# Optimization experiments

Hardware: AMD Instinct MI355X
Metric: run time of the kernel (lower is better)

Reference implementation:

```python
import jax, jax.numpy as jnp
from jax import lax
import numpy as np

EPS = 1e-5
TOPK_RATIO = 0.6

def _bn(y, gamma, beta, mean, var):
    # inference-mode BatchNorm3d over channel axis 1
    scale = gamma / jnp.sqrt(var + EPS)
    return (y - mean[None, :, None, None, None]) * scale[None, :, None, None, None] + beta[None, :, None, None, None]

def setup_inputs() -> dict:
    key = jax.random.key(0)
    ks = jax.random.split(key, 8)
    B, C, D, H, W = 4, 64, 16, 64, 64
    C8 = max(4, C // 8)  # bottleneck channels = 8
    x = jax.random.normal(ks[0], (B, C, D, H, W), dtype=jnp.float32)
    # depthwise conv weight, OIDHW with I=1 (groups=C), kernel (1,5,5)
    w_dw = jax.random.normal(ks[1], (C, 1, 1, 5, 5), dtype=jnp.float32) * 0.05
    bn1_gamma = jnp.ones((C,), jnp.float32)
    bn1_beta = jnp.zeros((C,), jnp.float32)
    bn1_mean = jax.random.normal(ks[2], (C,), jnp.float32) * 0.1
    bn1_var = jax.random.uniform(ks[3], (C,), jnp.float32, 0.5, 1.5)
    # pointwise 1x1x1 convs as matrices
    w_pw1 = jax.random.normal(ks[4], (C8, C), jnp.float32) * 0.05
    b_pw1 = jnp.zeros((C8,), jnp.float32)
    bn2_gamma = jnp.ones((C8,), jnp.float32)
    bn2_beta = jnp.zeros((C8,), jnp.float32)
    bn2_mean = jax.random.normal(ks[5], (C8,), jnp.float32) * 0.1
    bn2_var = jax.random.uniform(ks[6], (C8,), jnp.float32, 0.5, 1.5)
    w_pw2 = jax.random.normal(ks[7], (C, C8), jnp.float32) * 0.05
    b_pw2 = jnp.zeros((C,), jnp.float32)
    alpha = jnp.ones((), jnp.float32)
    return {"x": x, "w_dw": w_dw,
            "bn1_gamma": bn1_gamma, "bn1_beta": bn1_beta, "bn1_mean": bn1_mean, "bn1_var": bn1_var,
            "w_pw1": w_pw1, "b_pw1": b_pw1,
            "bn2_gamma": bn2_gamma, "bn2_beta": bn2_beta, "bn2_mean": bn2_mean, "bn2_var": bn2_var,
            "w_pw2": w_pw2, "b_pw2": b_pw2, "alpha": alpha}

def reference(x, w_dw, bn1_gamma, bn1_beta, bn1_mean, bn1_var,
              w_pw1, b_pw1, bn2_gamma, bn2_beta, bn2_mean, bn2_var,
              w_pw2, b_pw2, alpha):
    B, C, D, H, W = x.shape
    # branch1: depthwise conv3d (1,5,5), pad (0,2,2) + BN + SiLU
    y1 = lax.conv_general_dilated(
        x, w_dw, window_strides=(1, 1, 1),
        padding=((0, 0), (2, 2), (2, 2)),
        dimension_numbers=("NCDHW", "OIDHW", "NCDHW"),
        feature_group_count=C)
    y1 = jax.nn.silu(_bn(y1, bn1_gamma, bn1_beta, bn1_mean, bn1_var))
    # branch2: 1x1 conv -> BN -> SiLU -> 1x1 conv
    y2 = jnp.einsum("oc,bcdhw->bodhw", w_pw1, x) + b_pw1[None, :, None, None, None]
    y2 = jax.nn.silu(_bn(y2, bn2_gamma, bn2_beta, bn2_mean, bn2_var))
    y2 = jnp.einsum("oc,bcdhw->bodhw", w_pw2, y2) + b_pw2[None, :, None, None, None]
    attn = y1 * y2
    # channel-wise top-k threshold per spatial location
    k = max(1, int(TOPK_RATIO * C))
    attn_cl = jnp.moveaxis(attn, 1, -1)  # (B,D,H,W,C)
    thr = lax.top_k(attn_cl, k)[0][..., -1]  # k-th largest, (B,D,H,W)
    mask = (attn >= thr[:, None, :, :, :]).astype(attn.dtype)
    return x + alpha * (attn * mask)
```

## Files before the change

### kernel.cpp

```cpp
#include <hip/hip_runtime.h>
#include <hip/hip_fp16.h>

#define C  64
#define C8 8
#define EPSV 1e-5f

__device__ __forceinline__ float silu_f(float v) {
    return v * (1.f / (1.f + __expf(-v)));
}

__global__ __launch_bounds__(256) void fused_kernel(
    const float* __restrict__ x, const float* __restrict__ w_dw,
    const float* __restrict__ g1, const float* __restrict__ be1,
    const float* __restrict__ mu1, const float* __restrict__ va1,
    const float* __restrict__ w1, const float* __restrict__ b1,
    const float* __restrict__ g2, const float* __restrict__ be2,
    const float* __restrict__ mu2, const float* __restrict__ va2,
    const float* __restrict__ w2, const float* __restrict__ b2,
    const float* __restrict__ alphap, float* __restrict__ out)
{
    __shared__ __align__(16) __half y1s[C * 256];
    __shared__ __align__(16) __half xs [C * 256];

    const int blk = blockIdx.x;
    const int hb = blk & 15;
    const int d  = (blk >> 4) & 15;
    const int b  = blk >> 8;
    const int h0 = hb * 4;
    const int tid = threadIdx.x;

    {
        const int c     = tid >> 2;
        const int strip = tid & 3;
        const int w16   = strip * 16;
        const int q     = w16 >> 2;
        const int csw   = (c & 7) * 8;

        float wk[25];
#pragma unroll
        for (int i = 0; i < 25; ++i) wk[i] = w_dw[c * 25 + i];
        const float scale = g1[c] * rsqrtf(va1[c] + EPSV);
        const float shift = be1[c] - mu1[c] * scale;
        const long xbase = ((long)(b * C + c) * 16 + d) * 4096;

        float acc[4][16];
#pragma unroll
        for (int i = 0; i < 4; ++i)
#pragma unroll
            for (int ow = 0; ow < 16; ++ow) acc[i][ow] = 0.f;

#pragma unroll
        for (int j = 0; j < 8; ++j) {
            const int r = h0 + j - 2;
            if (r >= 0 && r < 64) {
                const float4* rowp = (const float4*)(x + xbase + r * 64);
                const float4 z = make_float4(0.f, 0.f, 0.f, 0.f);
                float4 u0 = (q > 0)  ? rowp[q - 1] : z;
                float4 u1 = rowp[q];
                float4 u2 = rowp[q + 1];
                float4 u3 = rowp[q + 2];
                float4 u4 = rowp[q + 3];
                float4 u5 = (q < 12) ? rowp[q + 4] : z;
                float vals[24] = {u0.x,u0.y,u0.z,u0.w, u1.x,u1.y,u1.z,u1.w,
                                  u2.x,u2.y,u2.z,u2.w, u3.x,u3.y,u3.z,u3.w,
                                  u4.x,u4.y,u4.z,u4.w, u5.x,u5.y,u5.z,u5.w};
                if (j >= 2 && j <= 5) {
                    const int i = j - 2;
                    const int chunkbase = i * 8 + 2 * strip;
#pragma unroll
                    for (int t = 0; t < 2; ++t) {
                        const int p = (chunkbase + t) ^ (c & 7);
                        union { __half2 h[4]; float4 f; } u;
#pragma unroll
                        for (int m = 0; m < 4; ++m)
                            u.h[m] = __floats2half2_rn(vals[4 + t * 8 + 2 * m],
                                                       vals[4 + t * 8 + 2 * m + 1]);
                        *(float4*)&xs[c * 256 + p * 8] = u.f;
                    }
                }
#pragma unroll
                for (int i = 0; i < 4; ++i) {
                    if (i <= j && (j - i) <= 4) {
                        const int kr = j - i;
#pragma unroll
                        for (int kc = 0; kc < 5; ++kc) {
                            const float kw = wk[kr * 5 + kc];
#pragma unroll
                            for (int ow = 0; ow < 16; ++ow)
                                acc[i][ow] += kw * vals[ow + kc + 2];
                        }
                    }
                }
            }
        }
#pragma unroll
        for (int i = 0; i < 4; ++i) {
            float o[16];
#pragma unroll
            for (int ow = 0; ow < 16; ++ow)
                o[ow] = silu_f(acc[i][ow] * scale + shift);
            const int chunkbase = i * 8 + 2 * strip;
#pragma unroll
            for (int t = 0; t < 2; ++t) {
                const int p = (chunkbase + t) ^ (c & 7);
                union { __half2 h[4]; float4 f; } u;
#pragma unroll
                for (int m = 0; m < 4; ++m)
                    u.h[m] = __floats2half2_rn(o[t * 8 + 2 * m], o[t * 8 + 2 * m + 1]);
                *(float4*)&y1s[c * 256 + p * 8] = u.f;
            }
        }
    }
    __syncthreads();

    {
        const int loc = tid;

        float s1[C8];
#pragma unroll
        for (int o = 0; o < C8; ++o) s1[o] = 0.f;
#pragma unroll
        for (int c = 0; c < C; ++c) {
            const float xc = __half2float(xs[c * 256 + (loc ^ ((c & 7) << 3))]);
#pragma unroll
            for (int o = 0; o < C8; ++o) s1[o] += w1[o * C + c] * xc;
        }
        float hh[C8];
#pragma unroll
        for (int o = 0; o < C8; ++o) {
            const float sc = g2[o] * rsqrtf(va2[o] + EPSV);
            hh[o] = silu_f((s1[o] + b1[o] - mu2[o]) * sc + be2[o]);
        }

        float a[C], t[C];
#pragma unroll
        for (int c = 0; c < C; ++c) {
            const float y1v = __half2float(y1s[c * 256 + (loc ^ ((c & 7) << 3))]);
            float y2 = b2[c];
#pragma unroll
            for (int o = 0; o < C8; ++o) y2 += w2[c * C8 + o] * hh[o];
            const float av = y1v * y2;
            a[c] = av;
            t[c] = av;
        }

#pragma unroll
        for (int k = 2; k <= 64; k <<= 1) {
#pragma unroll
            for (int j = k >> 1; j > 0; j >>= 1) {
#pragma unroll
                for (int i = 0; i < 64; ++i) {
                    const int l = i ^ j;
                    if (l > i) {
                        const float u = t[i], v = t[l];
                        const float mn = fminf(u, v), mx = fmaxf(u, v);
                        if ((i & k) == 0) { t[i] = mn; t[l] = mx; }
                        else              { t[i] = mx; t[l] = mn; }
                    }
                }
            }
        }
        const float thr = t[26];
        const float alpha = alphap[0];

        const int rg = d * 4096 + (h0 + (tid >> 6)) * 64 + (tid & 63);
        float* op = out + (long)b * (C * 65536) + rg;

#pragma unroll
        for (int c = 0; c < C; ++c) {
            const float xc = __half2float(xs[c * 256 + (loc ^ ((c & 7) << 3))]);
            const float av = a[c];
            op[(long)c * 65536] = xc + ((av >= thr) ? alpha * av : 0.f);
        }
    }
}

extern "C" void kernel_launch(void* const* d_in, const int* in_sizes, int n_in,
                              void* d_out, int out_size, void* d_ws, size_t ws_size,
                              hipStream_t stream) {
    const float* x    = (const float*)d_in[0];
    const float* w_dw = (const float*)d_in[1];
    const float* g1   = (const float*)d_in[2];
    const float* be1  = (const float*)d_in[3];
    const float* mu1  = (const float*)d_in[4];
    const float* va1  = (const float*)d_in[5];
    const float* w1   = (const float*)d_in[6];
    const float* b1   = (const float*)d_in[7];
    const float* g2   = (const float*)d_in[8];
    const float* be2  = (const float*)d_in[9];
    const float* mu2  = (const float*)d_in[10];
    const float* va2  = (const float*)d_in[11];
    const float* w2   = (const float*)d_in[12];
    const float* b2   = (const float*)d_in[13];
    const float* alp  = (const float*)d_in[14];
    float* out = (float*)d_out;

    fused_kernel<<<1024, 256, 0, stream>>>(
        x, w_dw, g1, be1, mu1, va1, w1, b1, g2, be2, mu2, va2, w2, b2, alp, out);
}
```

Before: 219.2 us.

## Cut registers and LDS: drop x staging, recompute attention, weights in LDS

Removes the fp16 shared-memory copy of x and rereads x from global memory (likely L2-resident) in the pointwise and output phases. The depthwise weights move from per-thread registers into a shared table. The attention values are recomputed in the output loop instead of being kept in a second 64-entry register array. Together with launch_bounds(256,4), this aims to lower VGPR and LDS use for higher occupancy. The trade is extra global loads and recomputed FMAs. Reading x at fp32 instead of from the fp16 copy also changes numerics slightly.

After: 386.2 us. 76.2% more time.

```diff
diff --git a/kernel.cpp b/kernel.cpp
--- a/kernel.cpp
+++ b/kernel.cpp
@@ -9,7 +9,7 @@
     return v * (1.f / (1.f + __expf(-v)));
 }
 
-__global__ __launch_bounds__(256) void fused_kernel(
+__global__ __launch_bounds__(256, 4) void fused_kernel(
     const float* __restrict__ x, const float* __restrict__ w_dw,
     const float* __restrict__ g1, const float* __restrict__ be1,
     const float* __restrict__ mu1, const float* __restrict__ va1,
@@ -20,7 +20,7 @@
     const float* __restrict__ alphap, float* __restrict__ out)
 {
     __shared__ __align__(16) __half y1s[C * 256];
-    __shared__ __align__(16) __half xs [C * 256];
+    __shared__ float wt[C * 25];
 
     const int blk = blockIdx.x;
     const int hb = blk & 15;
@@ -29,16 +29,15 @@
     const int h0 = hb * 4;
     const int tid = threadIdx.x;
 
+    for (int i = tid; i < C * 25; i += 256) wt[i] = w_dw[i];
+    __syncthreads();
+
     {
         const int c     = tid >> 2;
         const int strip = tid & 3;
         const int w16   = strip * 16;
         const int q     = w16 >> 2;
-        const int csw   = (c & 7) * 8;
 
-        float wk[25];
-#pragma unroll
-        for (int i = 0; i < 25; ++i) wk[i] = w_dw[c * 25 + i];
         const float scale = g1[c] * rsqrtf(va1[c] + EPSV);
         const float shift = be1[c] - mu1[c] * scale;
         const long xbase = ((long)(b * C + c) * 16 + d) * 4096;
@@ -64,27 +63,14 @@
                 float vals[24] = {u0.x,u0.y,u0.z,u0.w, u1.x,u1.y,u1.z,u1.w,
                                   u2.x,u2.y,u2.z,u2.w, u3.x,u3.y,u3.z,u3.w,
                                   u4.x,u4.y,u4.z,u4.w, u5.x,u5.y,u5.z,u5.w};
-                if (j >= 2 && j <= 5) {
-                    const int i = j - 2;
-                    const int chunkbase = i * 8 + 2 * strip;
-#pragma unroll
-                    for (int t = 0; t < 2; ++t) {
-                        const int p = (chunkbase + t) ^ (c & 7);
-                        union { __half2 h[4]; float4 f; } u;
-#pragma unroll
-                        for (int m = 0; m < 4; ++m)
-                            u.h[m] = __floats2half2_rn(vals[4 + t * 8 + 2 * m],
-                                                       vals[4 + t * 8 + 2 * m + 1]);
-                        *(float4*)&xs[c * 256 + p * 8] = u.f;
-                    }
-                }
 #pragma unroll
                 for (int i = 0; i < 4; ++i) {
                     if (i <= j && (j - i) <= 4) {
                         const int kr = j - i;
+                        const float* wrow = &wt[c * 25 + kr * 5];
 #pragma unroll
                         for (int kc = 0; kc < 5; ++kc) {
-                            const float kw = wk[kr * 5 + kc];
+                            const float kw = wrow[kc];
 #pragma unroll
                             for (int ow = 0; ow < 16; ++ow)
                                 acc[i][ow] += kw * vals[ow + kc + 2];
@@ -93,6 +79,7 @@
                 }
             }
         }
+        const int csw = (c & 7);
 #pragma unroll
         for (int i = 0; i < 4; ++i) {
             float o[16];
@@ -102,7 +89,7 @@
             const int chunkbase = i * 8 + 2 * strip;
 #pragma unroll
             for (int t = 0; t < 2; ++t) {
-                const int p = (chunkbase + t) ^ (c & 7);
+                const int p = (chunkbase + t) ^ csw;
                 union { __half2 h[4]; float4 f; } u;
 #pragma unroll
                 for (int m = 0; m < 4; ++m)
@@ -115,13 +102,15 @@
 
     {
         const int loc = tid;
+        const int rg  = d * 4096 + (h0 + (tid >> 6)) * 64 + (tid & 63);
+        const long xoff = (long)b * (C * 65536) + rg;
 
         float s1[C8];
 #pragma unroll
         for (int o = 0; o < C8; ++o) s1[o] = 0.f;
 #pragma unroll
         for (int c = 0; c < C; ++c) {
-            const float xc = __half2float(xs[c * 256 + (loc ^ ((c & 7) << 3))]);
+            const float xc = x[xoff + (long)c * 65536];
 #pragma unroll
             for (int o = 0; o < C8; ++o) s1[o] += w1[o * C + c] * xc;
         }
@@ -132,16 +121,14 @@
             hh[o] = silu_f((s1[o] + b1[o] - mu2[o]) * sc + be2[o]);
         }
 
-        float a[C], t[C];
+        float t[C];
 #pragma unroll
         for (int c = 0; c < C; ++c) {
             const float y1v = __half2float(y1s[c * 256 + (loc ^ ((c & 7) << 3))]);
             float y2 = b2[c];
 #pragma unroll
             for (int o = 0; o < C8; ++o) y2 += w2[c * C8 + o] * hh[o];
-            const float av = y1v * y2;
-            a[c] = av;
-            t[c] = av;
+            t[c] = y1v * y2;
         }
 
 #pragma unroll
@@ -163,13 +150,16 @@
         const float thr = t[26];
         const float alpha = alphap[0];
 
-        const int rg = d * 4096 + (h0 + (tid >> 6)) * 64 + (tid & 63);
-        float* op = out + (long)b * (C * 65536) + rg;
+        float* op = out + xoff;
 
 #pragma unroll
         for (int c = 0; c < C; ++c) {
-            const float xc = __half2float(xs[c * 256 + (loc ^ ((c & 7) << 3))]);
-            const float av = a[c];
+            const float y1v = __half2float(y1s[c * 256 + (loc ^ ((c & 7) << 3))]);
+            float y2 = b2[c];
+#pragma unroll
+            for (int o = 0; o < C8; ++o) y2 += w2[c * C8 + o] * hh[o];
+            const float av = y1v * y2;
+            const float xc = x[xoff + (long)c * 65536];
             op[(long)c * 65536] = xc + ((av >= thr) ? alpha * av : 0.f);
         }
     }
```

## Warp-specialize fused kernel into producer/consumer halves with double-buffered LDS

Applied to the files above, without the earlier changes.

Each block now runs 512 threads and covers four consecutive 4-row tiles. The first 256 threads compute the depthwise conv, BN and SiLU into one of two LDS buffers, while the other 256 threads handle the pointwise branch, top-k threshold and output store for the previous tile. The depthwise weights are staged in shared memory, and the consumer recomputes y2 at store time instead of keeping a second 64-entry array. This is meant to overlap the load-bound conv stage with the compute-heavy sort stage. In exchange it uses four times fewer blocks (256), doubles LDS per block, adds a pipeline fill and drain step, and introduces block-wide syncs every step.

Result: slower. 225.9 us (+3.1%).

```diff
diff --git a/kernel.cpp b/kernel.cpp
--- a/kernel.cpp
+++ b/kernel.cpp
@@ -3,13 +3,14 @@
 
 #define C  64
 #define C8 8
+#define NB 4
 #define EPSV 1e-5f
 
 __device__ __forceinline__ float silu_f(float v) {
     return v * (1.f / (1.f + __expf(-v)));
 }
 
-__global__ __launch_bounds__(256) void fused_kernel(
+__global__ __launch_bounds__(512) void fused_kernel(
     const float* __restrict__ x, const float* __restrict__ w_dw,
     const float* __restrict__ g1, const float* __restrict__ be1,
     const float* __restrict__ mu1, const float* __restrict__ va1,
@@ -19,159 +20,177 @@
     const float* __restrict__ w2, const float* __restrict__ b2,
     const float* __restrict__ alphap, float* __restrict__ out)
 {
-    __shared__ __align__(16) __half y1s[C * 256];
-    __shared__ __align__(16) __half xs [C * 256];
+    __shared__ __align__(16) __half y1s[2][C * 256];
+    __shared__ __align__(16) __half xs [2][C * 256];
+    __shared__ float wt[C * 25];
 
     const int blk = blockIdx.x;
-    const int hb = blk & 15;
-    const int d  = (blk >> 4) & 15;
-    const int b  = blk >> 8;
-    const int h0 = hb * 4;
+    const int hq  = blk & 3;
+    const int d   = (blk >> 2) & 15;
+    const int b   = blk >> 6;
     const int tid = threadIdx.x;
 
-    {
-        const int c     = tid >> 2;
-        const int strip = tid & 3;
-        const int w16   = strip * 16;
-        const int q     = w16 >> 2;
-        const int csw   = (c & 7) * 8;
-
-        float wk[25];
-#pragma unroll
-        for (int i = 0; i < 25; ++i) wk[i] = w_dw[c * 25 + i];
-        const float scale = g1[c] * rsqrtf(va1[c] + EPSV);
-        const float shift = be1[c] - mu1[c] * scale;
-        const long xbase = ((long)(b * C + c) * 16 + d) * 4096;
-
-        float acc[4][16];
-#pragma unroll
-        for (int i = 0; i < 4; ++i)
-#pragma unroll
-            for (int ow = 0; ow < 16; ++ow) acc[i][ow] = 0.f;
-
-#pragma unroll
-        for (int j = 0; j < 8; ++j) {
-            const int r = h0 + j - 2;
-            if (r >= 0 && r < 64) {
-                const float4* rowp = (const float4*)(x + xbase + r * 64);
-                const float4 z = make_float4(0.f, 0.f, 0.f, 0.f);
-                float4 u0 = (q > 0)  ? rowp[q - 1] : z;
-                float4 u1 = rowp[q];
-                float4 u2 = rowp[q + 1];
-                float4 u3 = rowp[q + 2];
-                float4 u4 = rowp[q + 3];
-                float4 u5 = (q < 12) ? rowp[q + 4] : z;
-                float vals[24] = {u0.x,u0.y,u0.z,u0.w, u1.x,u1.y,u1.z,u1.w,
-                                  u2.x,u2.y,u2.z,u2.w, u3.x,u3.y,u3.z,u3.w,
-                                  u4.x,u4.y,u4.z,u4.w, u5.x,u5.y,u5.z,u5.w};
-                if (j >= 2 && j <= 5) {
-                    const int i = j - 2;
-                    const int chunkbase = i * 8 + 2 * strip;
-#pragma unroll
-                    for (int t = 0; t < 2; ++t) {
-                        const int p = (chunkbase + t) ^ (c & 7);
-                        union { __half2 h[4]; float4 f; } u;
-#pragma unroll
-                        for (int m = 0; m < 4; ++m)
-                            u.h[m] = __floats2half2_rn(vals[4 + t * 8 + 2 * m],
-                                                       vals[4 + t * 8 + 2 * m + 1]);
-                        *(float4*)&xs[c * 256 + p * 8] = u.f;
-                    }
-                }
-#pragma unroll
-                for (int i = 0; i < 4; ++i) {
-                    if (i <= j && (j - i) <= 4) {
-                        const int kr = j - i;
-#pragma unroll
-                        for (int kc = 0; kc < 5; ++kc) {
-                            const float kw = wk[kr * 5 + kc];
-#pragma unroll
-                            for (int ow = 0; ow < 16; ++ow)
-                                acc[i][ow] += kw * vals[ow + kc + 2];
+    for (int i = tid; i < C * 25; i += 512) wt[i] = w_dw[i];
+    __syncthreads();
+
+    const bool producer = (tid < 256);
+
+    const int c     = (tid & 255) >> 2;
+    const int strip = tid & 3;
+    const int q     = (strip * 16) >> 2;
+    const int csw   = c & 7;
+    const float scale = g1[c] * rsqrtf(va1[c] + EPSV);
+    const float shift = be1[c] - mu1[c] * scale;
+    const long  xbase = ((long)(b * C + c) * 16 + d) * 4096;
+
+    const int ctid = tid & 255;
+
+    for (int k = 0; k <= NB; ++k) {
+        if (producer) {
+            if (k < NB) {
+                const int h0 = hq * 16 + k * 4;
+                __half* y1p = y1s[k & 1];
+                __half* xsp = xs [k & 1];
+
+                float acc[4][16];
+#pragma unroll
+                for (int i = 0; i < 4; ++i)
+#pragma unroll
+                    for (int ow = 0; ow < 16; ++ow) acc[i][ow] = 0.f;
+
+#pragma unroll
+                for (int j = 0; j < 8; ++j) {
+                    const int r = h0 + j - 2;
+                    if (r >= 0 && r < 64) {
+                        const float4* rowp = (const float4*)(x + xbase + r * 64);
+                        const float4 z = make_float4(0.f, 0.f, 0.f, 0.f);
+                        float4 u0 = (q > 0)  ? rowp[q - 1] : z;
+                        float4 u1 = rowp[q];
+                        float4 u2 = rowp[q + 1];
+                        float4 u3 = rowp[q + 2];
+                        float4 u4 = rowp[q + 3];
+                        float4 u5 = (q < 12) ? rowp[q + 4] : z;
+                        float vals[24] = {u0.x,u0.y,u0.z,u0.w, u1.x,u1.y,u1.z,u1.w,
+                                          u2.x,u2.y,u2.z,u2.w, u3.x,u3.y,u3.z,u3.w,
+                                          u4.x,u4.y,u4.z,u4.w, u5.x,u5.y,u5.z,u5.w};
+                        if (j >= 2 && j <= 5) {
+                            const int i = j - 2;
+                            const int chunkbase = i * 8 + 2 * strip;
+#pragma unroll
+                            for (int t = 0; t < 2; ++t) {
+                                const int p = (chunkbase + t) ^ csw;
+                                union { __half2 h[4]; float4 f; } u;
+#pragma unroll
+                                for (int m = 0; m < 4; ++m)
+                                    u.h[m] = __floats2half2_rn(vals[4 + t * 8 + 2 * m],
+                                                               vals[4 + t * 8 + 2 * m + 1]);
+                                *(float4*)&xsp[c * 256 + p * 8] = u.f;
+                            }
+                        }
+#pragma unroll
+                        for (int i = 0; i < 4; ++i) {
+                            if (i <= j && (j - i) <= 4) {
+                                const int kr = j - i;
+                                const float* wrow = &wt[c * 25 + kr * 5];
+#pragma unroll
+                                for (int kc = 0; kc < 5; ++kc) {
+                                    const float kw = wrow[kc];
+#pragma unroll
+                                    for (int ow = 0; ow < 16; ++ow)
+                                        acc[i][ow] += kw * vals[ow + kc + 2];
+                                }
+                            }
                         }
                     }
                 }
+#pragma unroll
+                for (int i = 0; i < 4; ++i) {
+                    float o[16];
+#pragma unroll
+                    for (int ow = 0; ow < 16; ++ow)
+                        o[ow] = silu_f(acc[i][ow] * scale + shift);
+                    const int chunkbase = i * 8 + 2 * strip;
+#pragma unroll
+                    for (int t = 0; t < 2; ++t) {
+                        const int p = (chunkbase + t) ^ csw;
+                        union { __half2 h[4]; float4 f; } u;
+#pragma unroll
+                        for (int m = 0; m < 4; ++m)
+                            u.h[m] = __floats2half2_rn(o[t * 8 + 2 * m],
+                                                       o[t * 8 + 2 * m + 1]);
+                        *(float4*)&y1p[c * 256 + p * 8] = u.f;
+                    }
+                }
+            }
+        } else {
+            if (k > 0) {
+                const int kk  = k - 1;
+                const int h0  = hq * 16 + kk * 4;
+                const __half* y1p = y1s[kk & 1];
+                const __half* xsp = xs [kk & 1];
+                const int loc = ctid;
+
+                float s1[C8];
+#pragma unroll
+                for (int o = 0; o < C8; ++o) s1[o] = 0.f;
+#pragma unroll
+                for (int cc = 0; cc < C; ++cc) {
+                    const float xc = __half2float(xsp[cc * 256 + (loc ^ ((cc & 7) << 3))]);
+#pragma unroll
+                    for (int o = 0; o < C8; ++o) s1[o] += w1[o * C + cc] * xc;
+                }
+                float hh[C8];
+#pragma unroll
+                for (int o = 0; o < C8; ++o) {
+                    const float sc = g2[o] * rsqrtf(va2[o] + EPSV);
+                    hh[o] = silu_f((s1[o] + b1[o] - mu2[o]) * sc + be2[o]);
+                }
+
+                float t[C];
+#pragma unroll
+                for (int cc = 0; cc < C; ++cc) {
+                    const float y1v = __half2float(y1p[cc * 256 + (loc ^ ((cc & 7) << 3))]);
+                    float y2 = b2[cc];
+#pragma unroll
+                    for (int o = 0; o < C8; ++o) y2 += w2[cc * C8 + o] * hh[o];
+                    t[cc] = y1v * y2;
+                }
+
+#pragma unroll
+                for (int kb = 2; kb <= 64; kb <<= 1) {
+#pragma unroll
+                    for (int j = kb >> 1; j > 0; j >>= 1) {
+#pragma unroll
+                        for (int i = 0; i < 64; ++i) {
+                            const int l = i ^ j;
+                            if (l > i) {
+                                const float u = t[i], v = t[l];
+                                const float mn = fminf(u, v), mx = fmaxf(u, v);
+                                if ((i & kb) == 0) { t[i] = mn; t[l] = mx; }
+                                else               { t[i] = mx; t[l] = mn; }
+                            }
+                        }
+                    }
+                }
+                const float thr = t[26];
+                const float alpha = alphap[0];
+
+                const int  rg   = d * 4096 + (h0 + (ctid >> 6)) * 64 + (ctid & 63);
+                const long ooff = (long)b * (C * 65536) + rg;
+
+#pragma unroll
+                for (int cc = 0; cc < C; ++cc) {
+                    const float y1v = __half2float(y1p[cc * 256 + (loc ^ ((cc & 7) << 3))]);
+                    float y2 = b2[cc];
+#pragma unroll
+                    for (int o = 0; o < C8; ++o) y2 += w2[cc * C8 + o] * hh[o];
+                    const float av = y1v * y2;
+                    const float xc = __half2float(xsp[cc * 256 + (loc ^ ((cc & 7) << 3))]);
+                    out[ooff + (long)cc * 65536] = xc + ((av >= thr) ? alpha * av : 0.f);
+                }
             }
         }
-#pragma unroll
-        for (int i = 0; i < 4; ++i) {
-            float o[16];
-#pragma unroll
-            for (int ow = 0; ow < 16; ++ow)
-                o[ow] = silu_f(acc[i][ow] * scale + shift);
-            const int chunkbase = i * 8 + 2 * strip;
-#pragma unroll
-            for (int t = 0; t < 2; ++t) {
-                const int p = (chunkbase + t) ^ (c & 7);
-                union { __half2 h[4]; float4 f; } u;
-#pragma unroll
-                for (int m = 0; m < 4; ++m)
-                    u.h[m] = __floats2half2_rn(o[t * 8 + 2 * m], o[t * 8 + 2 * m + 1]);
-                *(float4*)&y1s[c * 256 + p * 8] = u.f;
-            }
-        }
-    }
-    __syncthreads();
-
-    {
-        const int loc = tid;
-
-        float s1[C8];
-#pragma unroll
-        for (int o = 0; o < C8; ++o) s1[o] = 0.f;
-#pragma unroll
-        for (int c = 0; c < C; ++c) {
-            const float xc = __half2float(xs[c * 256 + (loc ^ ((c & 7) << 3))]);
-#pragma unroll
-            for (int o = 0; o < C8; ++o) s1[o] += w1[o * C + c] * xc;
-        }
-        float hh[C8];
-#pragma unroll
-        for (int o = 0; o < C8; ++o) {
-            const float sc = g2[o] * rsqrtf(va2[o] + EPSV);
-            hh[o] = silu_f((s1[o] + b1[o] - mu2[o]) * sc + be2[o]);
-        }
-
-        float a[C], t[C];
-#pragma unroll
-        for (int c = 0; c < C; ++c) {
-            const float y1v = __half2float(y1s[c * 256 + (loc ^ ((c & 7) << 3))]);
-            float y2 = b2[c];
-#pragma unroll
-            for (int o = 0; o < C8; ++o) y2 += w2[c * C8 + o] * hh[o];
-            const float av = y1v * y2;
-            a[c] = av;
-            t[c] = av;
-        }
-
-#pragma unroll
-        for (int k = 2; k <= 64; k <<= 1) {
-#pragma unroll
-            for (int j = k >> 1; j > 0; j >>= 1) {
-#pragma unroll
-                for (int i = 0; i < 64; ++i) {
-                    const int l = i ^ j;
-                    if (l > i) {
-                        const float u = t[i], v = t[l];
-                        const float mn = fminf(u, v), mx = fmaxf(u, v);
-                        if ((i & k) == 0) { t[i] = mn; t[l] = mx; }
-                        else              { t[i] = mx; t[l] = mn; }
-                    }
-                }
-            }
-        }
-        const float thr = t[26];
-        const float alpha = alphap[0];
-
-        const int rg = d * 4096 + (h0 + (tid >> 6)) * 64 + (tid & 63);
-        float* op = out + (long)b * (C * 65536) + rg;
-
-#pragma unroll
-        for (int c = 0; c < C; ++c) {
-            const float xc = __half2float(xs[c * 256 + (loc ^ ((c & 7) << 3))]);
-            const float av = a[c];
-            op[(long)c * 65536] = xc + ((av >= thr) ? alpha * av : 0.f);
-        }
+        __syncthreads();
     }
 }
 
@@ -195,6 +214,6 @@
     const float* alp  = (const float*)d_in[14];
     float* out = (float*)d_out;
 
-    fused_kernel<<<1024, 256, 0, stream>>>(
+    fused_kernel<<<256, 512, 0, stream>>>(
         x, w_dw, g1, be1, mu1, va1, w1, b1, g2, be2, mu2, va2, w2, b2, alp, out);
 }
```
